# Performance work log

Measured on AMD Instinct MI355X. Metric: run time of the kernel, lower is better.

## Reference

```python
import jax, jax.numpy as jnp
import numpy as np

N = 20000      # nodes
E = 320000     # edges
F = 128        # feat_dim
N_RBF = 20
CUTOFF = 5.0


def setup_inputs() -> dict:
    key = jax.random.key(0)
    ks = jax.random.split(key, 12)
    h_i = jax.random.normal(ks[0], (N, F), dtype=jnp.float32)
    v_i = jax.random.normal(ks[1], (N, F, 3), dtype=jnp.float32)
    # distances in (0, cutoff); keep strictly > 0 to avoid div-by-zero in sinc basis
    d_ij = (jax.random.uniform(ks[2], (E,), dtype=jnp.float32) * 0.98 + 0.01) * CUTOFF
    r = jax.random.normal(ks[3], (E, 3), dtype=jnp.float32)
    unit_r_ij = r / jnp.linalg.norm(r, axis=-1, keepdims=True)
    nbrs = jax.random.randint(ks[4], (E, 2), 0, N, dtype=jnp.int64)
    # params: layers = Dense(F->F, swish) then Dense(F->3F); dist_embed dense: n_rbf -> 3F
    s1 = 1.0 / np.sqrt(F)
    W1 = jax.random.uniform(ks[5], (F, F), jnp.float32, -s1, s1)
    b1 = jax.random.uniform(ks[6], (F,), jnp.float32, -s1, s1)
    W2 = jax.random.uniform(ks[7], (F, 3 * F), jnp.float32, -s1, s1)
    b2 = jax.random.uniform(ks[8], (3 * F,), jnp.float32, -s1, s1)
    sr = 1.0 / np.sqrt(N_RBF)
    Wr = jax.random.uniform(ks[9], (N_RBF, 3 * F), jnp.float32, -sr, sr)
    br = jax.random.uniform(ks[10], (3 * F,), jnp.float32, -sr, sr)
    return {"h_i": h_i, "v_i": v_i, "d_ij": d_ij, "unit_r_ij": unit_r_ij,
            "nbrs": nbrs, "W1": W1, "b1": b1, "W2": W2, "b2": b2, "Wr": Wr, "br": br}


def _dist_embed(d, Wr, br):
    # PaiNN sinc-like radial basis: sin(n*pi*d/cutoff)/d, n=1..N_RBF
    n = jnp.arange(1, N_RBF + 1, dtype=d.dtype)
    rbf = jnp.sin(n[None, :] * jnp.pi * d[:, None] / CUTOFF) / d[:, None]  # [E, N_RBF]
    # cosine cutoff envelope
    fcut = 0.5 * (jnp.cos(jnp.pi * d / CUTOFF) + 1.0) * (d < CUTOFF)       # [E]
    return (rbf @ Wr + br) * fcut[:, None]                                  # [E, 3F]


def reference(h_i, v_i, d_ij, unit_r_ij, nbrs, W1, b1, W2, b2, Wr, br):
    # phi = Dense(swish) -> Dense : [N, 3F]
    phi = jax.nn.silu(h_i @ W1 + b1) @ W2 + b2
    src = nbrs[:, 1]
    dst = nbrs[:, 0]
    edge_inv = phi[src] * _dist_embed(d_ij, Wr, br)          # [E, 3F]
    edge_inv = edge_inv.reshape(edge_inv.shape[0], 3, F)     # [E, 3, F]
    f1, f2, f3 = edge_inv[:, 0], edge_inv[:, 1], edge_inv[:, 2]
    # dv: [E, F, 3]
    dv = f1[:, :, None] * unit_r_ij[:, None, :] + f2[:, :, None] * v_i[src]
    dh_i = jax.ops.segment_sum(f3, dst, num_segments=N)      # [N, F]
    dv_i = jax.ops.segment_sum(dv, dst, num_segments=N)      # [N, F, 3]
    return (dh_i, dv_i)
```

## Files before the change

### kernel.cpp

```cpp
#include <hip/hip_runtime.h>
#include <math.h>

#define F 128
#define THREEF 384
#define N_RBF 20
#define CUTOFF 5.0f
#define CAP 64

__global__ __launch_bounds__(256) void mlp_kernel(
    const float* __restrict__ h, const float* __restrict__ W1,
    const float* __restrict__ b1, const float* __restrict__ W2,
    const float* __restrict__ b2, float* __restrict__ phi, int N)
{
    __shared__ float sh_h[16 * F];
    __shared__ float sh_t[16 * F];
    const int tid   = threadIdx.x;
    const int node0 = blockIdx.x * 16;

    {
        const float4* src = (const float4*)(h + (size_t)node0 * F);
        float4* dst = (float4*)sh_h;
        dst[tid]       = src[tid];
        dst[tid + 256] = src[tid + 256];
    }
    __syncthreads();

    const int j2 = tid & 63;
    const int r0 = (tid >> 6) * 4;

    {
        float acc[4][2];
        const float bb0 = b1[j2], bb1 = b1[j2 + 64];
        #pragma unroll
        for (int r = 0; r < 4; ++r) { acc[r][0] = bb0; acc[r][1] = bb1; }
        for (int k4 = 0; k4 < F; k4 += 4) {
            float4 a[4];
            #pragma unroll
            for (int r = 0; r < 4; ++r)
                a[r] = *(const float4*)&sh_h[(r0 + r) * F + k4];
            #pragma unroll
            for (int kk = 0; kk < 4; ++kk) {
                const float w0  = W1[(k4 + kk) * F + j2];
                const float w1v = W1[(k4 + kk) * F + j2 + 64];
                #pragma unroll
                for (int r = 0; r < 4; ++r) {
                    const float av = ((const float*)&a[r])[kk];
                    acc[r][0] = fmaf(av, w0,  acc[r][0]);
                    acc[r][1] = fmaf(av, w1v, acc[r][1]);
                }
            }
        }
        #pragma unroll
        for (int r = 0; r < 4; ++r) {
            const float x0 = acc[r][0], x1 = acc[r][1];
            sh_t[(r0 + r) * F + j2]      = x0 / (1.0f + __expf(-x0));
            sh_t[(r0 + r) * F + j2 + 64] = x1 / (1.0f + __expf(-x1));
        }
    }
    __syncthreads();

    {
        float acc[4][6];
        #pragma unroll
        for (int c = 0; c < 6; ++c) {
            const float bb = b2[j2 + c * 64];
            #pragma unroll
            for (int r = 0; r < 4; ++r) acc[r][c] = bb;
        }
        for (int k4 = 0; k4 < F; k4 += 4) {
            float4 a[4];
            #pragma unroll
            for (int r = 0; r < 4; ++r)
                a[r] = *(const float4*)&sh_t[(r0 + r) * F + k4];
            #pragma unroll
            for (int kk = 0; kk < 4; ++kk) {
                float w[6];
                #pragma unroll
                for (int c = 0; c < 6; ++c)
                    w[c] = W2[(k4 + kk) * THREEF + j2 + c * 64];
                #pragma unroll
                for (int r = 0; r < 4; ++r) {
                    const float av = ((const float*)&a[r])[kk];
                    #pragma unroll
                    for (int c = 0; c < 6; ++c)
                        acc[r][c] = fmaf(av, w[c], acc[r][c]);
                }
            }
        }
        #pragma unroll
        for (int r = 0; r < 4; ++r) {
            #pragma unroll
            for (int c = 0; c < 6; ++c) {
                const int col = j2 + c * 64;
                const int p   = col >> 7;
                const int fc  = col & 127;
                phi[(size_t)p * N * F + (size_t)(node0 + r0 + r) * F + fc] = acc[r][c];
            }
        }
    }
}

__global__ __launch_bounds__(256) void build_kernel(
    const float* __restrict__ d_ij, const float* __restrict__ unit_r,
    const int* __restrict__ nbrs, int* __restrict__ cnt,
    int* __restrict__ eid, float* __restrict__ pack, int E)
{
    int e = blockIdx.x * 256 + threadIdx.x;
    if (e >= E) return;
    const int dst = nbrs[2 * e];
    const int src = nbrs[2 * e + 1];
    const int slot = atomicAdd(&cnt[dst], 1);
    if (slot < CAP) eid[dst * CAP + slot] = e;

    const float d = d_ij[e];
    const float x = (float)M_PI * d * (1.0f / CUTOFF);
    float sx, cx;
    __sincosf(x, &sx, &cx);
    const float fcut = (d < CUTOFF) ? 0.5f * (cx + 1.0f) : 0.0f;
    float4 q0, q1;
    q0.x = sx * fcut / d;
    q0.y = 2.0f * cx;
    q0.z = fcut;
    q0.w = unit_r[3 * e + 0];
    q1.x = unit_r[3 * e + 1];
    q1.y = unit_r[3 * e + 2];
    q1.z = __int_as_float(src);
    q1.w = 0.0f;
    float4* pk = (float4*)(pack + (size_t)e * 8);
    pk[0] = q0;
    pk[1] = q1;
}

__global__ __launch_bounds__(128) void gather_kernel(
    const float* __restrict__ phi,
    const float* __restrict__ v_i,
    const float* __restrict__ Wr,
    const float* __restrict__ br,
    const int*   __restrict__ cnt,
    const int*   __restrict__ eid,
    const float* __restrict__ pack,
    float* __restrict__ dh,
    float* __restrict__ dv,
    int N)
{
    const int node = blockIdx.x;
    const int f    = threadIdx.x;

    const float br0 = br[f], br1 = br[f + 128], br2 = br[f + 256];

    const int deg0 = cnt[node];
    const int deg  = deg0 < CAP ? deg0 : CAP;
    const int* my_eid = eid + node * CAP;

    const float* phi0 = phi;
    const float* phi1 = phi + (size_t)N * F;
    const float* phi2 = phi + (size_t)2 * N * F;

    const float* wr0 = Wr + f;
    const float* wr1 = Wr + f + 128;
    const float* wr2 = Wr + f + 256;

    float dh_acc = 0.0f, dv0 = 0.0f, dv1 = 0.0f, dv2 = 0.0f;

    for (int i0 = 0; i0 < deg; i0 += 4) {
        float4 q0[4], q1[4];
        int    srcs[4];

        #pragma unroll
        for (int j = 0; j < 4; ++j) {
            const int idx = i0 + j;
            const int e = __builtin_amdgcn_readfirstlane(
                              my_eid[idx < deg ? idx : 0]);
            const float4* pkj = (const float4*)(pack + (size_t)e * 8);
            float4 a0 = pkj[0];
            float4 a1 = pkj[1];
            if (idx >= deg) { a0.x = 0.0f; a0.z = 0.0f; }
            q0[j] = a0;
            q1[j] = a1;
            srcs[j] = __builtin_amdgcn_readfirstlane(__float_as_int(a1.z));
        }

        float a[4][3], rp[4], rc[4], twoc[4];
        #pragma unroll
        for (int j = 0; j < 4; ++j) {
            const float fc = q0[j].z;
            a[j][0] = br0 * fc;
            a[j][1] = br1 * fc;
            a[j][2] = br2 * fc;
            rp[j]   = 0.0f;
            rc[j]   = q0[j].x;
            twoc[j] = q0[j].y;
        }

        #pragma unroll 4
        for (int n = 0; n < N_RBF; ++n) {
            const float w0 = wr0[n * THREEF];
            const float w1 = wr1[n * THREEF];
            const float w2 = wr2[n * THREEF];
            #pragma unroll
            for (int j = 0; j < 4; ++j) {
                a[j][0] = fmaf(rc[j], w0, a[j][0]);
                a[j][1] = fmaf(rc[j], w1, a[j][1]);
                a[j][2] = fmaf(rc[j], w2, a[j][2]);
                const float rn = fmaf(twoc[j], rc[j], -rp[j]);
                rp[j] = rc[j];
                rc[j] = rn;
            }
        }

        #pragma unroll
        for (int j = 0; j < 4; ++j) {
            const int src = srcs[j];
            const float f1 = phi0[(size_t)src * F + f] * a[j][0];
            const float f2 = phi1[(size_t)src * F + f] * a[j][1];
            const float f3 = phi2[(size_t)src * F + f] * a[j][2];

            dh_acc += f3;

            const float* vs = v_i + (size_t)src * THREEF + 3 * f;
            dv0 = fmaf(f1, q0[j].w, fmaf(f2, vs[0], dv0));
            dv1 = fmaf(f1, q1[j].x, fmaf(f2, vs[1], dv1));
            dv2 = fmaf(f1, q1[j].y, fmaf(f2, vs[2], dv2));
        }
    }

    dh[(size_t)node * F + f] = dh_acc;
    float* dvp = dv + (size_t)node * THREEF + 3 * f;
    dvp[0] = dv0;
    dvp[1] = dv1;
    dvp[2] = dv2;
}

extern "C" void kernel_launch(void* const* d_in, const int* in_sizes, int n_in,
                              void* d_out, int out_size, void* d_ws, size_t ws_size,
                              hipStream_t stream) {
    const float* h_i    = (const float*)d_in[0];
    const float* v_i    = (const float*)d_in[1];
    const float* d_ij   = (const float*)d_in[2];
    const float* unit_r = (const float*)d_in[3];
    const int*   nbrs   = (const int*)  d_in[4];
    const float* W1     = (const float*)d_in[5];
    const float* b1     = (const float*)d_in[6];
    const float* W2     = (const float*)d_in[7];
    const float* b2     = (const float*)d_in[8];
    const float* Wr     = (const float*)d_in[9];
    const float* br     = (const float*)d_in[10];

    const int N = in_sizes[0] / F;
    const int E = in_sizes[2];

    float* dh = (float*)d_out;
    float* dv = dh + (size_t)N * F;

    float* phi  = (float*)d_ws;
    float* pack = phi + (size_t)3 * N * F;
    int*   cnt  = (int*)(pack + (size_t)E * 8);
    int*   eid  = cnt + N;

    hipMemsetAsync(cnt, 0, (size_t)N * sizeof(int), stream);

    mlp_kernel<<<(N + 15) / 16, 256, 0, stream>>>(h_i, W1, b1, W2, b2, phi, N);
    build_kernel<<<(E + 255) / 256, 256, 0, stream>>>(d_ij, unit_r, nbrs, cnt,
                                                      eid, pack, E);
    gather_kernel<<<N, 128, 0, stream>>>(phi, v_i, Wr, br, cnt, eid, pack,
                                         dh, dv, N);
}
```

Baseline: 336.0 us.

## Stage Wr in LDS, pair nodes per gather block, enlarge MLP row tile

The gather kernel now copies the radial weight matrix Wr into shared memory once per block and handles two nodes per 256-thread block. This replaces repeated global loads of Wr inside the RBF loop. The MLP kernel processes 32 nodes per block, with 8 rows per thread, and splits the second GEMM into two 3-column passes, so each weight load is reused across more rows. Edge pack fields are now read as scalars instead of float4. Costs include a 30KB LDS fill per block, more register pressure, and N/2 launch assuming N is even.

New measurement: 355.4 us. 1.06x slower.

```diff
diff --git a/kernel.cpp b/kernel.cpp
--- a/kernel.cpp
+++ b/kernel.cpp
@@ -7,51 +7,58 @@
 #define CUTOFF 5.0f
 #define CAP 64
 
-__global__ __launch_bounds__(256) void mlp_kernel(
+__global__ __launch_bounds__(256, 2) void mlp_kernel(
     const float* __restrict__ h, const float* __restrict__ W1,
     const float* __restrict__ b1, const float* __restrict__ W2,
     const float* __restrict__ b2, float* __restrict__ phi, int N)
 {
-    __shared__ float sh_h[16 * F];
-    __shared__ float sh_t[16 * F];
+    __shared__ float sh_h[32 * F];
+    __shared__ float sh_t[32 * F];
     const int tid   = threadIdx.x;
-    const int node0 = blockIdx.x * 16;
+    const int node0 = blockIdx.x * 32;
 
     {
         const float4* src = (const float4*)(h + (size_t)node0 * F);
         float4* dst = (float4*)sh_h;
-        dst[tid]       = src[tid];
-        dst[tid + 256] = src[tid + 256];
+        #pragma unroll
+        for (int i = 0; i < 4; ++i)
+            dst[tid + i * 256] = src[tid + i * 256];
     }
     __syncthreads();
 
     const int j2 = tid & 63;
-    const int r0 = (tid >> 6) * 4;
+    const int r0 = (tid >> 6) * 8;
 
     {
-        float acc[4][2];
+        float acc[8][2];
         const float bb0 = b1[j2], bb1 = b1[j2 + 64];
         #pragma unroll
-        for (int r = 0; r < 4; ++r) { acc[r][0] = bb0; acc[r][1] = bb1; }
+        for (int r = 0; r < 8; ++r) { acc[r][0] = bb0; acc[r][1] = bb1; }
         for (int k4 = 0; k4 < F; k4 += 4) {
-            float4 a[4];
-            #pragma unroll
-            for (int r = 0; r < 4; ++r)
-                a[r] = *(const float4*)&sh_h[(r0 + r) * F + k4];
+            float w[4][2];
             #pragma unroll
             for (int kk = 0; kk < 4; ++kk) {
-                const float w0  = W1[(k4 + kk) * F + j2];
-                const float w1v = W1[(k4 + kk) * F + j2 + 64];
-                #pragma unroll
-                for (int r = 0; r < 4; ++r) {
-                    const float av = ((const float*)&a[r])[kk];
-                    acc[r][0] = fmaf(av, w0,  acc[r][0]);
-                    acc[r][1] = fmaf(av, w1v, acc[r][1]);
-                }
-            }
-        }
-        #pragma unroll
-        for (int r = 0; r < 4; ++r) {
+                w[kk][0] = W1[(k4 + kk) * F + j2];
+                w[kk][1] = W1[(k4 + kk) * F + j2 + 64];
+            }
+            #pragma unroll
+            for (int half = 0; half < 2; ++half) {
+                float4 a[4];
+                #pragma unroll
+                for (int r = 0; r < 4; ++r)
+                    a[r] = *(const float4*)&sh_h[(r0 + half * 4 + r) * F + k4];
+                #pragma unroll
+                for (int kk = 0; kk < 4; ++kk)
+                    #pragma unroll
+                    for (int r = 0; r < 4; ++r) {
+                        const float av = ((const float*)&a[r])[kk];
+                        acc[half * 4 + r][0] = fmaf(av, w[kk][0], acc[half * 4 + r][0]);
+                        acc[half * 4 + r][1] = fmaf(av, w[kk][1], acc[half * 4 + r][1]);
+                    }
+            }
+        }
+        #pragma unroll
+        for (int r = 0; r < 8; ++r) {
             const float x0 = acc[r][0], x1 = acc[r][1];
             sh_t[(r0 + r) * F + j2]      = x0 / (1.0f + __expf(-x0));
             sh_t[(r0 + r) * F + j2 + 64] = x1 / (1.0f + __expf(-x1));
@@ -59,44 +66,50 @@
     }
     __syncthreads();
 
-    {
-        float acc[4][6];
-        #pragma unroll
-        for (int c = 0; c < 6; ++c) {
-            const float bb = b2[j2 + c * 64];
-            #pragma unroll
-            for (int r = 0; r < 4; ++r) acc[r][c] = bb;
+    #pragma unroll
+    for (int pass = 0; pass < 2; ++pass) {
+        const int c0 = pass * 3;
+        float acc[8][3];
+        #pragma unroll
+        for (int c = 0; c < 3; ++c) {
+            const float bb = b2[j2 + (c0 + c) * 64];
+            #pragma unroll
+            for (int r = 0; r < 8; ++r) acc[r][c] = bb;
         }
         for (int k4 = 0; k4 < F; k4 += 4) {
-            float4 a[4];
-            #pragma unroll
-            for (int r = 0; r < 4; ++r)
-                a[r] = *(const float4*)&sh_t[(r0 + r) * F + k4];
-            #pragma unroll
-            for (int kk = 0; kk < 4; ++kk) {
-                float w[6];
-                #pragma unroll
-                for (int c = 0; c < 6; ++c)
-                    w[c] = W2[(k4 + kk) * THREEF + j2 + c * 64];
-                #pragma unroll
-                for (int r = 0; r < 4; ++r) {
-                    const float av = ((const float*)&a[r])[kk];
+            float w[4][3];
+            #pragma unroll
+            for (int kk = 0; kk < 4; ++kk)
+                #pragma unroll
+                for (int c = 0; c < 3; ++c)
+                    w[kk][c] = W2[(k4 + kk) * THREEF + j2 + (c0 + c) * 64];
+            #pragma unroll
+            for (int half = 0; half < 2; ++half) {
+                float4 a[4];
+                #pragma unroll
+                for (int r = 0; r < 4; ++r)
+                    a[r] = *(const float4*)&sh_t[(r0 + half * 4 + r) * F + k4];
+                #pragma unroll
+                for (int kk = 0; kk < 4; ++kk)
                     #pragma unroll
-                    for (int c = 0; c < 6; ++c)
-                        acc[r][c] = fmaf(av, w[c], acc[r][c]);
-                }
-            }
-        }
-        #pragma unroll
-        for (int r = 0; r < 4; ++r) {
-            #pragma unroll
-            for (int c = 0; c < 6; ++c) {
-                const int col = j2 + c * 64;
+                    for (int r = 0; r < 4; ++r) {
+                        const float av = ((const float*)&a[r])[kk];
+                        #pragma unroll
+                        for (int c = 0; c < 3; ++c)
+                            acc[half * 4 + r][c] =
+                                fmaf(av, w[kk][c], acc[half * 4 + r][c]);
+                    }
+            }
+        }
+        #pragma unroll
+        for (int r = 0; r < 8; ++r)
+            #pragma unroll
+            for (int c = 0; c < 3; ++c) {
+                const int col = j2 + (c0 + c) * 64;
                 const int p   = col >> 7;
                 const int fc  = col & 127;
                 phi[(size_t)p * N * F + (size_t)(node0 + r0 + r) * F + fc] = acc[r][c];
             }
-        }
     }
 }
 
@@ -131,7 +144,7 @@
     pk[1] = q1;
 }
 
-__global__ __launch_bounds__(128) void gather_kernel(
+__global__ __launch_bounds__(256, 2) void gather_kernel(
     const float* __restrict__ phi,
     const float* __restrict__ v_i,
     const float* __restrict__ Wr,
@@ -143,8 +156,22 @@
     float* __restrict__ dv,
     int N)
 {
-    const int node = blockIdx.x;
-    const int f    = threadIdx.x;
+    __shared__ float sWr[N_RBF * THREEF];
+
+    const int tid = threadIdx.x;
+    {
+        float4* dws = (float4*)sWr;
+        const float4* wsrc = (const float4*)Wr;
+        #pragma unroll
+        for (int i = 0; i < 8; ++i) {
+            const int idx = tid + i * 256;
+            if (idx < N_RBF * THREEF / 4) dws[idx] = wsrc[idx];
+        }
+    }
+    __syncthreads();
+
+    const int node = blockIdx.x * 2 + (tid >> 7);
+    const int f    = tid & 127;
 
     const float br0 = br[f], br1 = br[f + 128], br2 = br[f + 256];
 
@@ -155,53 +182,52 @@
     const float* phi0 = phi;
     const float* phi1 = phi + (size_t)N * F;
     const float* phi2 = phi + (size_t)2 * N * F;
-
-    const float* wr0 = Wr + f;
-    const float* wr1 = Wr + f + 128;
-    const float* wr2 = Wr + f + 256;
+    const float* wf   = sWr + f;
 
     float dh_acc = 0.0f, dv0 = 0.0f, dv1 = 0.0f, dv2 = 0.0f;
 
     for (int i0 = 0; i0 < deg; i0 += 4) {
-        float4 q0[4], q1[4];
-        int    srcs[4];
-
+        float s1[4], twoc[4], fcut[4], ux[4], uy[4], uz[4];
+        int   srcs[4];
         #pragma unroll
         for (int j = 0; j < 4; ++j) {
             const int idx = i0 + j;
             const int e = __builtin_amdgcn_readfirstlane(
-                              my_eid[idx < deg ? idx : 0]);
-            const float4* pkj = (const float4*)(pack + (size_t)e * 8);
-            float4 a0 = pkj[0];
-            float4 a1 = pkj[1];
-            if (idx >= deg) { a0.x = 0.0f; a0.z = 0.0f; }
-            q0[j] = a0;
-            q1[j] = a1;
-            srcs[j] = __builtin_amdgcn_readfirstlane(__float_as_int(a1.z));
-        }
-
-        float a[4][3], rp[4], rc[4], twoc[4];
+                              my_eid[idx < deg ? idx : i0]);
+            const float* pkj = pack + (size_t)e * 8;
+            float s  = pkj[0];
+            twoc[j]  = pkj[1];
+            float fc = pkj[2];
+            ux[j]    = pkj[3];
+            uy[j]    = pkj[4];
+            uz[j]    = pkj[5];
+            srcs[j]  = __builtin_amdgcn_readfirstlane(
+                           __float_as_int(pkj[6]));
+            if (idx >= deg) { s = 0.0f; fc = 0.0f; }
+            s1[j] = s;
+            fcut[j] = fc;
+        }
+
+        float a0[4], a1[4], a2[4], rp[4], rc[4];
         #pragma unroll
         for (int j = 0; j < 4; ++j) {
-            const float fc = q0[j].z;
-            a[j][0] = br0 * fc;
-            a[j][1] = br1 * fc;
-            a[j][2] = br2 * fc;
-            rp[j]   = 0.0f;
-            rc[j]   = q0[j].x;
-            twoc[j] = q0[j].y;
-        }
-
-        #pragma unroll 4
+            a0[j] = br0 * fcut[j];
+            a1[j] = br1 * fcut[j];
+            a2[j] = br2 * fcut[j];
+            rp[j] = 0.0f;
+            rc[j] = s1[j];
+        }
+
+        #pragma unroll
         for (int n = 0; n < N_RBF; ++n) {
-            const float w0 = wr0[n * THREEF];
-            const float w1 = wr1[n * THREEF];
-            const float w2 = wr2[n * THREEF];
+            const float w0 = wf[n * THREEF];
+            const float w1 = wf[n * THREEF + 128];
+            const float w2 = wf[n * THREEF + 256];
             #pragma unroll
             for (int j = 0; j < 4; ++j) {
-                a[j][0] = fmaf(rc[j], w0, a[j][0]);
-                a[j][1] = fmaf(rc[j], w1, a[j][1]);
-                a[j][2] = fmaf(rc[j], w2, a[j][2]);
+                a0[j] = fmaf(rc[j], w0, a0[j]);
+                a1[j] = fmaf(rc[j], w1, a1[j]);
+                a2[j] = fmaf(rc[j], w2, a2[j]);
                 const float rn = fmaf(twoc[j], rc[j], -rp[j]);
                 rp[j] = rc[j];
                 rc[j] = rn;
@@ -211,16 +237,16 @@
         #pragma unroll
         for (int j = 0; j < 4; ++j) {
             const int src = srcs[j];
-            const float f1 = phi0[(size_t)src * F + f] * a[j][0];
-            const float f2 = phi1[(size_t)src * F + f] * a[j][1];
-            const float f3 = phi2[(size_t)src * F + f] * a[j][2];
+            const float f1 = phi0[(size_t)src * F + f] * a0[j];
+            const float f2 = phi1[(size_t)src * F + f] * a1[j];
+            const float f3 = phi2[(size_t)src * F + f] * a2[j];
 
             dh_acc += f3;
 
             const float* vs = v_i + (size_t)src * THREEF + 3 * f;
-            dv0 = fmaf(f1, q0[j].w, fmaf(f2, vs[0], dv0));
-            dv1 = fmaf(f1, q1[j].x, fmaf(f2, vs[1], dv1));
-            dv2 = fmaf(f1, q1[j].y, fmaf(f2, vs[2], dv2));
+            dv0 = fmaf(f1, ux[j], fmaf(f2, vs[0], dv0));
+            dv1 = fmaf(f1, uy[j], fmaf(f2, vs[1], dv1));
+            dv2 = fmaf(f1, uz[j], fmaf(f2, vs[2], dv2));
         }
     }
 
@@ -259,9 +285,9 @@
 
     hipMemsetAsync(cnt, 0, (size_t)N * sizeof(int), stream);
 
-    mlp_kernel<<<(N + 15) / 16, 256, 0, stream>>>(h_i, W1, b1, W2, b2, phi, N);
+    mlp_kernel<<<(N + 31) / 32, 256, 0, stream>>>(h_i, W1, b1, W2, b2, phi, N);
     build_kernel<<<(E + 255) / 256, 256, 0, stream>>>(d_ij, unit_r, nbrs, cnt,
                                                       eid, pack, E);
-    gather_kernel<<<N, 128, 0, stream>>>(phi, v_i, Wr, br, cnt, eid, pack,
-                                         dh, dv, N);
-}
+    gather_kernel<<<N / 2, 256, 0, stream>>>(phi, v_i, Wr, br, cnt, eid, pack,
+                                             dh, dv, N);
+}
```
